# Kernel optimization log

Measured on AMD Instinct MI355X. Metric: run time of the kernel, lower is better.

Reference implementation:

```python
import jax, jax.numpy as jnp
import numpy as np

BSZ, N, E, D = 8, 1024, 49152, 256
K, ALPHA = 10, 0.1
EDGE_RATIO, NODE_RATIO = 0.8, 0.7
K_NODES = int(np.ceil(NODE_RATIO * N))  # torch_geometric topk uses ceil -> 717


def setup_inputs() -> dict:
    key = jax.random.key(0)
    ks = jax.random.split(key, 10)
    concept_hidden = jax.random.normal(ks[0], (BSZ, N, D), jnp.float32)
    head = jax.random.randint(ks[1], (BSZ, E), 0, N, jnp.int32)
    off = jax.random.randint(ks[2], (BSZ, E), 1, N, jnp.int32)
    tail = ((head + off) % N).astype(jnp.int32)  # guaranteed no self-loops
    triple_label = jnp.ones((BSZ, E), jnp.int32)  # all edges valid (no -1 padding)
    relation_hidden = jnp.zeros((BSZ, 1), jnp.float32)  # unused by the math
    concept_labels = jax.random.randint(ks[3], (BSZ, N), 0, 3, jnp.int32)
    concept_ids = jax.random.randint(ks[4], (BSZ, N), 0, 50000, jnp.int32)
    # PageRank temp (learnable param, deterministic init from alpha/K)
    t = ALPHA * (1.0 - ALPHA) ** np.arange(K + 1)
    t[-1] = (1.0 - ALPHA) ** K
    temp = jnp.asarray(t, jnp.float32)
    # GraphAttention params (heads=1)
    g = float(np.sqrt(6.0 / (D + D)))
    W_proj = jax.random.uniform(ks[5], (D, D), jnp.float32, -g, g)
    ga = float(np.sqrt(6.0 / (1 + D)))
    a_src = jax.random.uniform(ks[6], (D,), jnp.float32, -ga, ga)
    a_tgt = jax.random.uniform(ks[7], (D,), jnp.float32, -ga, ga)
    # output Linear(2D -> D)
    gl = float(np.sqrt(1.0 / (2 * D)))
    W_lin = jax.random.uniform(ks[8], (D, 2 * D), jnp.float32, -gl, gl)
    b_lin = jax.random.uniform(ks[9], (D,), jnp.float32, -gl, gl)
    return dict(concept_hidden=concept_hidden, relation_hidden=relation_hidden,
                head=head, tail=tail, triple_label=triple_label,
                concept_labels=concept_labels, concept_ids=concept_ids,
                temp=temp, W_proj=W_proj, a_src=a_src, a_tgt=a_tgt,
                W_lin=W_lin, b_lin=b_lin)


def _per_sample(x, h, t, labels, ids, temp, W_proj, a_src, a_tgt, W_lin, b_lin):
    # ---- PageRank (gcn_norm with added self-loops, aggr='add' into tail) ----
    sl = jnp.arange(N, dtype=jnp.int32)
    hs = jnp.concatenate([h, sl])
    ts = jnp.concatenate([t, sl])
    deg = jax.ops.segment_sum(jnp.ones(E + N, x.dtype), ts, num_segments=N)
    dinv = jnp.where(deg > 0, jax.lax.rsqrt(deg), 0.0)
    norm = dinv[hs] * dinv[ts]  # [E+N]

    def step(xk, gamma):
        xk = jax.ops.segment_sum(norm[:, None] * xk[hs], ts, num_segments=N)
        return xk, gamma * xk

    _, contribs = jax.lax.scan(step, x, temp[1:])  # K steps
    x_cut = temp[0] * x + contribs.sum(0)  # [N, D]

    # ---- edge attention (GAT-style scoring, sigmoid) ----
    proj = x_cut @ W_proj.T                       # [N, D] (heads=1)
    s_src = proj @ a_src                          # [N]
    s_tgt = proj @ a_tgt                          # [N]
    attn = jax.nn.sigmoid(s_src[h] + s_tgt[t])    # [E]

    # ---- symmetrize + coalesce(mean), done densely ----
    rows = jnp.concatenate([h, t])
    cols = jnp.concatenate([t, h])
    vals = jnp.concatenate([attn, attn])
    S = jnp.zeros((N, N), x.dtype).at[rows, cols].add(vals)
    Cn = jnp.zeros((N, N), x.dtype).at[rows, cols].add(1.0)
    valid = Cn > 0
    A = jnp.where(valid, S / jnp.maximum(Cn, 1.0), 0.0)  # coalesced mean adjacency

    # ---- np.percentile(attn, 20) with linear interpolation over valid edges ----
    sv = jnp.sort(jnp.where(valid, A, jnp.inf).reshape(-1))  # valid values first
    M = valid.sum()
    pos = (1.0 - EDGE_RATIO) * (M.astype(x.dtype) - 1.0)
    lo = jnp.floor(pos).astype(jnp.int32)
    frac = pos - lo.astype(x.dtype)
    hi = jnp.minimum(lo + 1, M - 1)  # stays within the finite (valid) prefix
    cut = sv[lo] + frac * (sv[hi] - sv[lo])

    A_cut = jnp.where(valid & (A >= cut), A, 0.0)  # edges below percentile zeroed

    # ---- node scoring: scatter_add of attn*x[src] into dst == A_cut^T @ x ----
    out = A_cut.T @ x                              # [N, D]
    score = jnp.abs(out).sum(1) + 1e-7             # [N]
    _, perm = jax.lax.top_k(score, K_NODES)

    pooled = A_cut[perm] @ x                       # [k, D]
    hcat = jnp.concatenate([x[perm], pooled], axis=-1)  # [k, 2D]
    h_new = hcat @ W_lin.T + b_lin                 # [k, D]
    return h_new, labels[perm], ids[perm]


def reference(concept_hidden, relation_hidden, head, tail, triple_label,
              concept_labels, concept_ids, temp, W_proj, a_src, a_tgt,
              W_lin, b_lin):
    f = jax.vmap(_per_sample,
                 in_axes=(0, 0, 0, 0, 0, None, None, None, None, None, None))
    return f(concept_hidden, head, tail, concept_labels, concept_ids,
             temp, W_proj, a_src, a_tgt, W_lin, b_lin)
```

## Files before the change

kernel.cpp:

```cpp
#include <hip/hip_runtime.h>
#include <math.h>

#define BSZ 8
#define NN 1024
#define EE 49152
#define DD 256
#define KSTEPS 10
#define NCH 192
#define KNODES 717
#define RS 256
#define MROWS 720

typedef __attribute__((ext_vector_type(8))) short short8_t;
typedef __attribute__((ext_vector_type(4))) float f32x4;

__device__ __forceinline__ void fma4(float4& a, float w, const float4 v) {
    a.x += w * v.x; a.y += w * v.y; a.z += w * v.z; a.w += w * v.w;
}

__device__ __forceinline__ unsigned short f2bf(float f) {
    unsigned u = __float_as_uint(f);
    u = (u + 0x7fffu + ((u >> 16) & 1u)) >> 16;
    return (unsigned short)u;
}


__global__ void k_hist(const int* __restrict__ head, const int* __restrict__ tail,
                       int* __restrict__ cnt_t, int* __restrict__ cnt_h) {
    __shared__ int lt[NN];
    __shared__ int lh[NN];
    int b = blockIdx.x / NCH, ch = blockIdx.x % NCH;
    int tid = threadIdx.x;
    for (int i = tid; i < NN; i += 256) { lt[i] = 0; lh[i] = 0; }
    __syncthreads();
    int e = ch * 256 + tid;
    int h = head[b * EE + e], t = tail[b * EE + e];
    atomicAdd(&lt[t], 1);
    atomicAdd(&lh[h], 1);
    __syncthreads();
    int base = (b * NCH + ch) * NN;
    for (int i = tid; i < NN; i += 256) { cnt_t[base + i] = lt[i]; cnt_h[base + i] = lh[i]; }
}

__global__ void k_chunkscan(int* __restrict__ cnt_t, int* __restrict__ cnt_h,
                            int* __restrict__ tot_t, int* __restrict__ tot_h,
                            float* __restrict__ dinv) {
    int gid = blockIdx.x * 256 + threadIdx.x;
    int which = gid >> 13;
    int i = gid & 8191;
    int b = i >> 10, n = i & 1023;
    int* c = which ? cnt_h : cnt_t;
    int run = 0;
    for (int s = 0; s < NCH; s++) {
        int idx = (b * NCH + s) * NN + n;
        int v = c[idx];
        c[idx] = run;
        run += v;
    }
    (which ? tot_h : tot_t)[i] = run;
    if (!which) dinv[i] = 1.0f / sqrtf((float)(run + 1));
}

__global__ __launch_bounds__(1024) void k_nodescan(const int* __restrict__ tot_t,
                                                   const int* __restrict__ tot_h,
                                                   int* __restrict__ toff, int* __restrict__ hoff) {
    __shared__ int sb[NN];
    int b = blockIdx.x >> 1, which = blockIdx.x & 1;
    int tid = threadIdx.x;
    const int* tot = which ? tot_h : tot_t;
    int* off = which ? hoff : toff;
    int v = tot[b * NN + tid];
    sb[tid] = v;
    __syncthreads();
    for (int o = 1; o < NN; o <<= 1) {
        int t = (tid >= o) ? sb[tid - o] : 0;
        __syncthreads();
        sb[tid] += t;
        __syncthreads();
    }
    off[b * (NN + 1) + tid] = sb[tid] - v;
    if (tid == NN - 1) off[b * (NN + 1) + NN] = sb[tid];
}

__global__ void k_fill(const int* __restrict__ head, const int* __restrict__ tail,
                       const int* __restrict__ cnt_t, const int* __restrict__ cnt_h,
                       const int* __restrict__ toff, const int* __restrict__ hoff,
                       const float* __restrict__ dinv,
                       int* __restrict__ t_head, float* __restrict__ t_norm, int* __restrict__ t_eidx,
                       int* __restrict__ h_tail, int* __restrict__ h_eidx) {
    __shared__ int sh[256], st[256];
    int b = blockIdx.x / NCH, ch = blockIdx.x % NCH;
    int tid = threadIdx.x;
    int e = ch * 256 + tid;
    int h = head[b * EE + e], t = tail[b * EE + e];
    sh[tid] = h;
    st[tid] = t;
    __syncthreads();
    int rt = 0, rh = 0;
    for (int j = 0; j < tid; j++) {
        rt += (st[j] == t);
        rh += (sh[j] == h);
    }
    int post = toff[b * (NN + 1) + t] + cnt_t[(b * NCH + ch) * NN + t] + rt;
    t_head[b * EE + post] = h;
    t_norm[b * EE + post] = dinv[b * NN + h] * dinv[b * NN + t];
    t_eidx[b * EE + post] = e;
    int posh = hoff[b * (NN + 1) + h] + cnt_h[(b * NCH + ch) * NN + h] + rh;
    h_tail[b * EE + posh] = t;
    h_eidx[b * EE + posh] = e;
}

__global__ __launch_bounds__(256) void k_prstep(const float* __restrict__ src, float* __restrict__ dst,
                         float* __restrict__ xacc, const float* __restrict__ temp,
                         const int* __restrict__ toff, const int* __restrict__ t_head,
                         const float* __restrict__ t_norm, const float* __restrict__ dinv,
                         int kidx) {
    int wid = threadIdx.x >> 6, lane = threadIdx.x & 63;
    int b = blockIdx.x & 7;
    int n = (blockIdx.x >> 3) * 4 + wid;
    int g = b * NN + n;
    int o0 = __builtin_amdgcn_readfirstlane(toff[b * (NN + 1) + n]);
    int o1 = __builtin_amdgcn_readfirstlane(toff[b * (NN + 1) + n + 1]);
    int ebase = __builtin_amdgcn_readfirstlane(b * EE);
    const int* __restrict__ hp = t_head + ebase;
    const float* __restrict__ wp = t_norm + ebase;
    float dv = dinv[g];
    const float4* src4 = (const float4*)src;
    size_t r4 = (size_t)g * 64 + lane;
    size_t bb = (size_t)b * NN * 64;
    float4 sv = src4[r4];
    float sl = dv * dv;
    float4 acc;
    acc.x = sl * sv.x; acc.y = sl * sv.y; acc.z = sl * sv.z; acc.w = sl * sv.w;
    int j = o0;
    for (; j + 8 <= o1; j += 8) {
        int c0 = hp[j], c1 = hp[j + 1], c2 = hp[j + 2], c3 = hp[j + 3];
        int c4 = hp[j + 4], c5 = hp[j + 5], c6 = hp[j + 6], c7 = hp[j + 7];
        float w0 = wp[j], w1 = wp[j + 1], w2 = wp[j + 2], w3 = wp[j + 3];
        float w4 = wp[j + 4], w5 = wp[j + 5], w6 = wp[j + 6], w7 = wp[j + 7];
        float4 xa = src4[bb + (size_t)c0 * 64 + lane];
        float4 xb = src4[bb + (size_t)c1 * 64 + lane];
        float4 xc = src4[bb + (size_t)c2 * 64 + lane];
        float4 xd = src4[bb + (size_t)c3 * 64 + lane];
        float4 xe = src4[bb + (size_t)c4 * 64 + lane];
        float4 xf = src4[bb + (size_t)c5 * 64 + lane];
        float4 xg = src4[bb + (size_t)c6 * 64 + lane];
        float4 xh = src4[bb + (size_t)c7 * 64 + lane];
        fma4(acc, w0, xa); fma4(acc, w1, xb); fma4(acc, w2, xc); fma4(acc, w3, xd);
        fma4(acc, w4, xe); fma4(acc, w5, xf); fma4(acc, w6, xg); fma4(acc, w7, xh);
    }
    for (; j + 4 <= o1; j += 4) {
        int c0 = hp[j], c1 = hp[j + 1], c2 = hp[j + 2], c3 = hp[j + 3];
        float w0 = wp[j], w1 = wp[j + 1], w2 = wp[j + 2], w3 = wp[j + 3];
        float4 xa = src4[bb + (size_t)c0 * 64 + lane];
        float4 xb = src4[bb + (size_t)c1 * 64 + lane];
        float4 xc = src4[bb + (size_t)c2 * 64 + lane];
        float4 xd = src4[bb + (size_t)c3 * 64 + lane];
        fma4(acc, w0, xa); fma4(acc, w1, xb); fma4(acc, w2, xc); fma4(acc, w3, xd);
    }
    for (; j < o1; j++) {
        int c0 = hp[j];
        float w0 = wp[j];
        float4 xa = src4[bb + (size_t)c0 * 64 + lane];
        fma4(acc, w0, xa);
    }
    ((float4*)dst)[r4] = acc;
    float gm = temp[kidx + 1];
    float4 xa2;
    if (kidx == 0) {
        float t0 = temp[0];
        xa2.x = t0 * sv.x; xa2.y = t0 * sv.y; xa2.z = t0 * sv.z; xa2.w = t0 * sv.w;
    } else {
        xa2 = ((float4*)xacc)[r4];
    }
    fma4(xa2, gm, acc);
    ((float4*)xacc)[r4] = xa2;
}


__global__ void k_vsrc(const float* __restrict__ Wp, const float* __restrict__ as_,
                       const float* __restrict__ at_, float* __restrict__ vsrc,
                       float* __restrict__ vtgt) {
    int d = threadIdx.x;
    float vs = 0.f, vt = 0.f;
    for (int i = 0; i < DD; i++) {
        float w = Wp[i * DD + d];
        vs += as_[i] * w;
        vt += at_[i] * w;
    }
    vsrc[d] = vs;
    vtgt[d] = vt;
}

__global__ void k_s(const float* __restrict__ xacc, const float* __restrict__ vsrc,
                    const float* __restrict__ vtgt, float* __restrict__ ssrc,
                    float* __restrict__ stgt) {
    int g = blockIdx.x * 4 + (threadIdx.x >> 6);
    int lane = threadIdx.x & 63;
    const float4* xr = (const float4*)(xacc + (size_t)g * DD);
    float4 xv = xr[lane];
    float4 vs = ((const float4*)vsrc)[lane];
    float4 vt = ((const float4*)vtgt)[lane];
    float s1 = xv.x * vs.x + xv.y * vs.y + xv.z * vs.z + xv.w * vs.w;
    float s2 = xv.x * vt.x + xv.y * vt.y + xv.z * vt.z + xv.w * vt.w;
    for (int o = 32; o > 0; o >>= 1) {
        s1 += __shfl_down(s1, o);
        s2 += __shfl_down(s2, o);
    }
    if (lane == 0) {
        ssrc[g] = s1;
        stgt[g] = s2;
    }
}

__global__ void k_attn(const int* __restrict__ head, const int* __restrict__ tail,
                       const float* __restrict__ ssrc, const float* __restrict__ stgt,
                       float* __restrict__ attn) {
    int i = blockIdx.x * 256 + threadIdx.x;
    int b = i / EE;
    int h = head[i], t = tail[i];
    float z = ssrc[b * NN + h] + stgt[b * NN + t];
    attn[i] = 1.0f / (1.0f + expf(-z));
}


__global__ __launch_bounds__(256) void k_rowbuild(const int* __restrict__ hoff, const int* __restrict__ h_tail,
                          const int* __restrict__ h_eidx, const int* __restrict__ toff,
                          const int* __restrict__ t_head, const int* __restrict__ t_eidx,
                          const float* __restrict__ attn,
                          int* __restrict__ rcol, float* __restrict__ rval,
                          int* __restrict__ nnzrow) {
    __shared__ int cols[RS];
    __shared__ float vals[RS];
    __shared__ int first[NN];
    __shared__ int cntb[NN];
    __shared__ int rankv[NN];
    __shared__ int ssum[256];
    int g = blockIdx.x;
    int b = g >> 10, n = g & 1023;
    int tid = threadIdx.x;
    int a0 = hoff[b * (NN + 1) + n], a1 = hoff[b * (NN + 1) + n + 1];
    int c0 = toff[b * (NN + 1) + n], c1 = toff[b * (NN + 1) + n + 1];
    int kh = a1 - a0;
    int kk = kh + (c1 - c0);
    if (kk > RS) kk = RS;
    for (int i = tid; i < NN; i += 256) { first[i] = 0x7fffffff; cntb[i] = 0; }
    __syncthreads();
    if (tid < kk) {
        int c, e;
        if (tid < kh) { c = h_tail[b * EE + a0 + tid]; e = h_eidx[b * EE + a0 + tid]; }
        else          { c = t_head[b * EE + c0 + (tid - kh)]; e = t_eidx[b * EE + c0 + (tid - kh)]; }
        cols[tid] = c;
        vals[tid] = attn[b * EE + e];
        atomicMin(&first[c], tid);
        atomicAdd(&cntb[c], 1);
    }
    __syncthreads();
    int i0 = tid * 4;
    int p0 = (first[i0] != 0x7fffffff);
    int p1 = (first[i0 + 1] != 0x7fffffff);
    int p2 = (first[i0 + 2] != 0x7fffffff);
    int p3 = (first[i0 + 3] != 0x7fffffff);
    int psum = p0 + p1 + p2 + p3;
    ssum[tid] = psum;
    __syncthreads();
    for (int o = 1; o < 256; o <<= 1) {
        int t = (tid >= o) ? ssum[tid - o] : 0;
        __syncthreads();
        ssum[tid] += t;
        __syncthreads();
    }
    int run = ssum[tid] - psum;
    rankv[i0] = run;            run += p0;
    rankv[i0 + 1] = run;        run += p1;
    rankv[i0 + 2] = run;        run += p2;
    rankv[i0 + 3] = run;
    int total = ssum[255];
    __syncthreads();
    if (tid < kk) {
        int c = cols[tid];
        if (first[c] == tid) {
            int cc = cntb[c];
            float v;
            if (cc == 1) {
                v = vals[tid];
            } else {
                float s = 0.f;
                for (int j = tid; j < kk; j++)
                    if (cols[j] == c) s += vals[j];
                v = s / (float)cc;
            }
            size_t rb = ((size_t)g << 8) + rankv[c];
            rcol[rb] = c;
            rval[rb] = v;
        }
    }
    if (tid == 0) nnzrow[g] = total;
}

__global__ void k_msum(const int* __restrict__ nnzrow, int* __restrict__ Mcnt) {
    __shared__ int red[256];
    int b = blockIdx.x, tid = threadIdx.x;
    int s = nnzrow[b * NN + tid] + nnzrow[b * NN + 256 + tid] +
            nnzrow[b * NN + 512 + tid] + nnzrow[b * NN + 768 + tid];
    red[tid] = s;
    __syncthreads();
    for (int o = 128; o > 0; o >>= 1) {
        if (tid < o) red[tid] += red[tid + o];
        __syncthreads();
    }
    if (tid == 0) Mcnt[b] = red[0];
}


__global__ void k_selinit(const int* __restrict__ Mcnt, int* __restrict__ sel) {
    int b = threadIdx.x;
    if (b < BSZ) {
        int M = Mcnt[b];
        float pos = 0.2f * ((float)M - 1.0f);
        int lo = (int)floorf(pos);
        float frac = pos - (float)lo;
        sel[b * 8 + 0] = lo;
        sel[b * 8 + 1] = min(lo + 1, M - 1);
        sel[b * 8 + 2] = 0;
        sel[b * 8 + 3] = 0;
        sel[b * 8 + 4] = __float_as_int(frac);
    }
}

__global__ void k_selhist(const float* __restrict__ rv, const int* __restrict__ sel,
                          int* __restrict__ hist, int pass) {
    __shared__ int lh[512];
    int tid = threadIdx.x;
    lh[tid] = 0;
    lh[tid + 256] = 0;
    __syncthreads();
    size_t base = (size_t)blockIdx.x * 1024;
    int b = blockIdx.x >> 8;
    unsigned p0 = (unsigned)sel[b * 8 + 2];
    unsigned p1 = (unsigned)sel[b * 8 + 3];
    int shift = 24 - 8 * pass;
    for (int u = 0; u < 4; u++) {
        float a = rv[base + u * 256 + tid];
        if (a > 0.f) {
            unsigned bits = __float_as_uint(a);
            unsigned bucket = (bits >> shift) & 255u;
            if (pass == 0) {
                atomicAdd(&lh[bucket], 1);
                atomicAdd(&lh[256 + bucket], 1);
            } else {
                unsigned hibits = bits >> (shift + 8);
                if (hibits == p0) atomicAdd(&lh[bucket], 1);
                if (hibits == p1) atomicAdd(&lh[256 + bucket], 1);
            }
        }
    }
    __syncthreads();
    int v0 = lh[tid];
    if (v0) atomicAdd(&hist[(b * 2 + 0) * 256 + tid], v0);
    int v1 = lh[tid + 256];
    if (v1) atomicAdd(&hist[(b * 2 + 1) * 256 + tid], v1);
}

__global__ void k_selreduce(int* __restrict__ hist, int* __restrict__ sel) {
    __shared__ int sb[256];
    int b = blockIdx.x >> 1, ch = blockIdx.x & 1;
    int tid = threadIdx.x;
    int idx = (b * 2 + ch) * 256 + tid;
    int v = hist[idx];
    hist[idx] = 0;
    int rem = sel[b * 8 + ch];
    int pref = sel[b * 8 + 2 + ch];
    sb[tid] = v;
    __syncthreads();
    for (int o = 1; o < 256; o <<= 1) {
        int t = (tid >= o) ? sb[tid - o] : 0;
        __syncthreads();
        sb[tid] += t;
        __syncthreads();
    }
    int excl = sb[tid] - v;
    if (v > 0 && rem >= excl && rem < excl + v) {
        sel[b * 8 + ch] = rem - excl;
        sel[b * 8 + 2 + ch] = (pref << 8) | tid;
    }
}

__global__ void k_cut(const int* __restrict__ sel, float* __restrict__ cut) {
    int b = threadIdx.x;
    if (b < BSZ) {
        float v0 = __uint_as_float((unsigned)sel[b * 8 + 2]);
        float v1 = __uint_as_float((unsigned)sel[b * 8 + 3]);
        float frac = __int_as_float(sel[b * 8 + 4]);
        cut[b] = v0 + frac * (v1 - v0);
    }
}


__global__ __launch_bounds__(256) void k_outscore(const int* __restrict__ rcol, const float* __restrict__ rval,
                           const int* __restrict__ nnzrow, const float* __restrict__ x,
                           const float* __restrict__ cut, float* __restrict__ out_pr,
                           float* __restrict__ score) {
    int wid = threadIdx.x >> 6, lane = threadIdx.x & 63;
    int b = blockIdx.x & 7;
    int n = (blockIdx.x >> 3) * 4 + wid;
    int g = b * NN + n;
    float cb = cut[b];
    int nnz = __builtin_amdgcn_readfirstlane(nnzrow[g]);
    int rbase = __builtin_amdgcn_readfirstlane(g << 8);
    const int* __restrict__ cp = rcol + rbase;
    const float* __restrict__ vp = rval + rbase;
    const float4* x4 = (const float4*)x;
    size_t bb = (size_t)b * NN * 64;
    float4 acc = make_float4(0.f, 0.f, 0.f, 0.f);
    int j = 0;
    for (; j + 4 <= nnz; j += 4) {
        float a0 = vp[j], a1 = vp[j + 1], a2 = vp[j + 2], a3 = vp[j + 3];
        int c0 = cp[j], c1 = cp[j + 1], c2 = cp[j + 2], c3 = cp[j + 3];
        float4 xa = x4[bb + (size_t)c0 * 64 + lane];
        float4 xb = x4[bb + (size_t)c1 * 64 + lane];
        float4 xc = x4[bb + (size_t)c2 * 64 + lane];
        float4 xd = x4[bb + (size_t)c3 * 64 + lane];
        if (a0 >= cb) fma4(acc, a0, xa);
        if (a1 >= cb) fma4(acc, a1, xb);
        if (a2 >= cb) fma4(acc, a2, xc);
        if (a3 >= cb) fma4(acc, a3, xd);
    }
    for (; j < nnz; j++) {
        float a0 = vp[j];
        int c0 = cp[j];
        float4 xa = x4[bb + (size_t)c0 * 64 + lane];
        if (a0 >= cb) fma4(acc, a0, xa);
    }
    ((float4*)out_pr)[(size_t)g * 64 + lane] = acc;
    float4 r;
    r.x = fabsf(acc.x); r.y = fabsf(acc.y); r.z = fabsf(acc.z); r.w = fabsf(acc.w);
    for (int o = 32; o > 0; o >>= 1) {
        r.x += __shfl_down(r.x, o);
        r.y += __shfl_down(r.y, o);
        r.z += __shfl_down(r.z, o);
        r.w += __shfl_down(r.w, o);
    }
    r.x += r.z;
    r.y += r.w;
    r.x += r.y;
    if (lane == 0) score[g] = r.x + 1e-7f;
}


__global__ __launch_bounds__(1024) void k_topk(const float* __restrict__ score,
                                               const int* __restrict__ labels,
                                               const int* __restrict__ ids,
                                               int* __restrict__ perm,
                                               float* __restrict__ out_lab,
                                               float* __restrict__ out_ids) {
    __shared__ float sc[NN];
    __shared__ int idx[NN];
    int b = blockIdx.x, tid = threadIdx.x;
    sc[tid] = score[b * NN + tid];
    idx[tid] = tid;
    __syncthreads();
    for (int k = 2; k <= NN; k <<= 1) {
        for (int j = k >> 1; j > 0; j >>= 1) {
            int p = tid ^ j;
            if (p > tid) {
                float s0 = sc[tid], s1 = sc[p];
                int i0 = idx[tid], i1 = idx[p];
                bool before01 = (s0 > s1) || (s0 == s1 && i0 < i1);
                bool up = ((tid & k) == 0);
                bool sw = up ? (!before01) : before01;
                if (sw) {
                    sc[tid] = s1; sc[p] = s0;
                    idx[tid] = i1; idx[p] = i0;
                }
            }
            __syncthreads();
        }
    }
    perm[b * NN + tid] = idx[tid];
    if (tid < KNODES) {
        int p = idx[tid];
        out_lab[b * KNODES + tid] = (float)labels[b * NN + p];
        out_ids[b * KNODES + tid] = (float)ids[b * NN + p];
    }
}


__global__ void k_wbf16(const float* __restrict__ W, unsigned short* __restrict__ Wb) {
    int i = blockIdx.x * 256 + threadIdx.x;
    Wb[i] = f2bf(W[i]);
}

__global__ void k_packA(const float* __restrict__ x, const float* __restrict__ outpr,
                        const int* __restrict__ perm, unsigned short* __restrict__ A16) {
    int row = blockIdx.x;
    int b = row / MROWS, i = row - b * MROWS;
    int tid = threadIdx.x;
    size_t ob = (size_t)row * 512;
    if (i < KNODES) {
        int p = perm[b * NN + i];
        float v0 = x[((size_t)(b * NN + p)) * DD + tid];
        float v1 = outpr[((size_t)(b * NN + p)) * DD + tid];
        A16[ob + tid] = f2bf(v0);
        A16[ob + 256 + tid] = f2bf(v1);
    } else {
        A16[ob + tid] = 0;
        A16[ob + 256 + tid] = 0;
    }
}

__global__ __launch_bounds__(256) void k_hnew_mfma(const unsigned short* __restrict__ A16,
                                                   const unsigned short* __restrict__ Wb,
                                                   const float* __restrict__ b_lin,
                                                   float* __restrict__ hnew) {
    int w = blockIdx.x * 4 + (threadIdx.x >> 6);
    int lane = threadIdx.x & 63;
    int b = w / (45 * 16);
    int rem = w - b * (45 * 16);
    int mt = rem >> 4, nt = rem & 15;
    int m = lane & 15, quad = lane >> 4;
    const unsigned short* ap = A16 + ((size_t)(b * MROWS + mt * 16 + m) * 512 + quad * 8);
    const unsigned short* bp = Wb + ((size_t)(nt * 16 + m) * 512 + quad * 8);
    f32x4 acc = {0.f, 0.f, 0.f, 0.f};
#pragma unroll
    for (int s = 0; s < 16; s++) {
        short8_t av = *(const short8_t*)(ap + s * 32);
        short8_t bv = *(const short8_t*)(bp + s * 32);
        acc = __builtin_amdgcn_mfma_f32_16x16x32_bf16(av, bv, acc, 0, 0, 0);
    }
    int d = nt * 16 + m;
    float bl = b_lin[d];
#pragma unroll
    for (int r = 0; r < 4; r++) {
        int i = mt * 16 + quad * 4 + r;
        if (i < KNODES) hnew[((size_t)(b * KNODES + i)) * DD + d] = acc[r] + bl;
    }
}


extern "C" void kernel_launch(void* const* d_in, const int* in_sizes, int n_in,
                              void* d_out, int out_size, void* d_ws, size_t ws_size,
                              hipStream_t stream) {
    const float* x      = (const float*)d_in[0];
    const int*   head   = (const int*)d_in[2];
    const int*   tail   = (const int*)d_in[3];
    const int*   labels = (const int*)d_in[5];
    const int*   ids    = (const int*)d_in[6];
    const float* temp   = (const float*)d_in[7];
    const float* Wp     = (const float*)d_in[8];
    const float* asrc   = (const float*)d_in[9];
    const float* atgt   = (const float*)d_in[10];
    const float* Wl     = (const float*)d_in[11];
    const float* blin   = (const float*)d_in[12];

    float* out_h   = (float*)d_out;
    float* out_lab = out_h + (size_t)BSZ * KNODES * DD;
    float* out_ids = out_lab + (size_t)BSZ * KNODES;

    size_t o = 0;
    char* ws = (char*)d_ws;
    auto A_ = [&](size_t bytes) -> void* {
        void* p = ws + o;
        o += (bytes + 255) & ~(size_t)255;
        return p;
    };
    int*   cnt_t  = (int*)  A_((size_t)BSZ * NCH * NN * 4);
    int*   cnt_h  = (int*)  A_((size_t)BSZ * NCH * NN * 4);
    int*   tot_t  = (int*)  A_((size_t)BSZ * NN * 4);
    int*   tot_h  = (int*)  A_((size_t)BSZ * NN * 4);
    int*   toff   = (int*)  A_((size_t)BSZ * (NN + 1) * 4);
    int*   hoff   = (int*)  A_((size_t)BSZ * (NN + 1) * 4);
    float* dinv   = (float*)A_((size_t)BSZ * NN * 4);
    int*   t_head = (int*)  A_((size_t)BSZ * EE * 4);
    float* t_norm = (float*)A_((size_t)BSZ * EE * 4);
    int*   t_eidx = (int*)  A_((size_t)BSZ * EE * 4);
    int*   h_tail = (int*)  A_((size_t)BSZ * EE * 4);
    int*   h_eidx = (int*)  A_((size_t)BSZ * EE * 4);
    float* xkA    = (float*)A_((size_t)BSZ * NN * DD * 4);
    float* xkB    = (float*)A_((size_t)BSZ * NN * DD * 4);
    float* xacc   = (float*)A_((size_t)BSZ * NN * DD * 4);
    float* vsrc   = (float*)A_(DD * 4);
    float* vtgt   = (float*)A_(DD * 4);
    float* ssrc   = (float*)A_((size_t)BSZ * NN * 4);
    float* stgt   = (float*)A_((size_t)BSZ * NN * 4);
    float* attn   = (float*)A_((size_t)BSZ * EE * 4);
    int*   rcol   = (int*)  A_((size_t)BSZ * NN * RS * 4);
    float* rval   = (float*)A_((size_t)BSZ * NN * RS * 4);
    int*   nnzrow = (int*)  A_((size_t)BSZ * NN * 4);
    int*   Mcnt   = (int*)  A_(BSZ * 4);
    int*   sel    = (int*)  A_(BSZ * 8 * 4);
    int*   hist   = (int*)  A_(BSZ * 2 * 256 * 4);
    float* cutv   = (float*)A_(BSZ * 4);
    float* outpr  = (float*)A_((size_t)BSZ * NN * DD * 4);
    float* scorev = (float*)A_((size_t)BSZ * NN * 4);
    int*   perm   = (int*)  A_((size_t)BSZ * NN * 4);
    unsigned short* Wb16 = (unsigned short*)A_((size_t)DD * 512 * 2);
    unsigned short* A16  = (unsigned short*)A_((size_t)BSZ * MROWS * 512 * 2);
    if (o > ws_size) return;

    hipMemsetAsync(rval, 0, (size_t)BSZ * NN * RS * 4, stream);
    hipMemsetAsync(hist, 0, BSZ * 2 * 256 * 4, stream);

    k_wbf16<<<DD * 512 / 256, 256, 0, stream>>>(Wl, Wb16);
    k_hist<<<BSZ * NCH, 256, 0, stream>>>(head, tail, cnt_t, cnt_h);
    k_chunkscan<<<64, 256, 0, stream>>>(cnt_t, cnt_h, tot_t, tot_h, dinv);
    k_nodescan<<<16, 1024, 0, stream>>>(tot_t, tot_h, toff, hoff);
    k_fill<<<BSZ * NCH, 256, 0, stream>>>(head, tail, cnt_t, cnt_h, toff, hoff, dinv,
                                          t_head, t_norm, t_eidx, h_tail, h_eidx);
    for (int k = 0; k < KSTEPS; k++) {
        const float* src = (k == 0) ? x : ((k & 1) ? xkA : xkB);
        float* dst = (k & 1) ? xkB : xkA;
        k_prstep<<<BSZ * NN / 4, 256, 0, stream>>>(src, dst, xacc, temp, toff, t_head, t_norm, dinv, k);
    }
    k_vsrc<<<1, 256, 0, stream>>>(Wp, asrc, atgt, vsrc, vtgt);
    k_s<<<BSZ * NN / 4, 256, 0, stream>>>(xacc, vsrc, vtgt, ssrc, stgt);
    k_attn<<<BSZ * EE / 256, 256, 0, stream>>>(head, tail, ssrc, stgt, attn);
    k_rowbuild<<<BSZ * NN, 256, 0, stream>>>(hoff, h_tail, h_eidx, toff, t_head, t_eidx,
                                             attn, rcol, rval, nnzrow);
    k_msum<<<BSZ, 256, 0, stream>>>(nnzrow, Mcnt);
    k_selinit<<<1, 64, 0, stream>>>(Mcnt, sel);
    for (int p = 0; p < 4; p++) {
        k_selhist<<<BSZ * 256, 256, 0, stream>>>(rval, sel, hist, p);
        k_selreduce<<<16, 256, 0, stream>>>(hist, sel);
    }
    k_cut<<<1, 64, 0, stream>>>(sel, cutv);
    k_outscore<<<BSZ * NN / 4, 256, 0, stream>>>(rcol, rval, nnzrow, x, cutv, outpr, scorev);
    k_topk<<<BSZ, 1024, 0, stream>>>(scorev, labels, ids, perm, out_lab, out_ids);
    k_packA<<<BSZ * MROWS, 256, 0, stream>>>(x, outpr, perm, A16);
    k_hnew_mfma<<<BSZ * 45 * 16 / 4, 256, 0, stream>>>(A16, Wb16, blin, out_h);
}
```

Before: 465.3 us.

## Fuse small kernels, compact percentile values, single-kernel radix select, fuse packA into topk

Folds the W_lin bf16 conversion into k_hist and the vsrc computation into the last PageRank step as extra blocks. k_rowbuild now appends each row's values to a compact per-batch buffer through an atomic base. This lets one block-per-batch k_select replace the msum/selinit/4×(selhist+selreduce)/cut launch chain and removes the large rval memset. The PR gather loop is unrolled to 16, and A16 packing moves into k_topk. It saves many launches and the full rval scans, but the select and packing now run on only 8 blocks, which limits parallelism.

```diff
diff --git a/kernel.cpp b/kernel.cpp
--- a/kernel.cpp
+++ b/kernel.cpp
@@ -10,6 +10,7 @@
 #define KNODES 717
 #define RS 256
 #define MROWS 720
+#define CSTRIDE 131072
 
 typedef __attribute__((ext_vector_type(8))) short short8_t;
 typedef __attribute__((ext_vector_type(4))) float f32x4;
@@ -26,11 +27,17 @@
 
 
 __global__ void k_hist(const int* __restrict__ head, const int* __restrict__ tail,
-                       int* __restrict__ cnt_t, int* __restrict__ cnt_h) {
+                       int* __restrict__ cnt_t, int* __restrict__ cnt_h,
+                       const float* __restrict__ Wl, unsigned short* __restrict__ Wb) {
     __shared__ int lt[NN];
     __shared__ int lh[NN];
+    int tid = threadIdx.x;
+    if (blockIdx.x >= BSZ * NCH) {
+        int i = (blockIdx.x - BSZ * NCH) * 256 + tid;
+        Wb[i] = f2bf(Wl[i]);
+        return;
+    }
     int b = blockIdx.x / NCH, ch = blockIdx.x % NCH;
-    int tid = threadIdx.x;
     for (int i = tid; i < NN; i += 256) { lt[i] = 0; lh[i] = 0; }
     __syncthreads();
     int e = ch * 256 + tid;
@@ -114,7 +121,22 @@
                          float* __restrict__ xacc, const float* __restrict__ temp,
                          const int* __restrict__ toff, const int* __restrict__ t_head,
                          const float* __restrict__ t_norm, const float* __restrict__ dinv,
-                         int kidx) {
+                         int kidx,
+                         const float* __restrict__ Wp, const float* __restrict__ as_,
+                         const float* __restrict__ at_, float* __restrict__ vsrc,
+                         float* __restrict__ vtgt) {
+    if (blockIdx.x >= BSZ * NN / 4) {
+        int d = threadIdx.x;
+        float vs = 0.f, vt = 0.f;
+        for (int i = 0; i < DD; i++) {
+            float w = Wp[i * DD + d];
+            vs += as_[i] * w;
+            vt += at_[i] * w;
+        }
+        vsrc[d] = vs;
+        vtgt[d] = vt;
+        return;
+    }
     int wid = threadIdx.x >> 6, lane = threadIdx.x & 63;
     int b = blockIdx.x & 7;
     int n = (blockIdx.x >> 3) * 4 + wid;
@@ -133,21 +155,17 @@
     float4 acc;
     acc.x = sl * sv.x; acc.y = sl * sv.y; acc.z = sl * sv.z; acc.w = sl * sv.w;
     int j = o0;
-    for (; j + 8 <= o1; j += 8) {
-        int c0 = hp[j], c1 = hp[j + 1], c2 = hp[j + 2], c3 = hp[j + 3];
-        int c4 = hp[j + 4], c5 = hp[j + 5], c6 = hp[j + 6], c7 = hp[j + 7];
-        float w0 = wp[j], w1 = wp[j + 1], w2 = wp[j + 2], w3 = wp[j + 3];
-        float w4 = wp[j + 4], w5 = wp[j + 5], w6 = wp[j + 6], w7 = wp[j + 7];
-        float4 xa = src4[bb + (size_t)c0 * 64 + lane];
-        float4 xb = src4[bb + (size_t)c1 * 64 + lane];
-        float4 xc = src4[bb + (size_t)c2 * 64 + lane];
-        float4 xd = src4[bb + (size_t)c3 * 64 + lane];
-        float4 xe = src4[bb + (size_t)c4 * 64 + lane];
-        float4 xf = src4[bb + (size_t)c5 * 64 + lane];
-        float4 xg = src4[bb + (size_t)c6 * 64 + lane];
-        float4 xh = src4[bb + (size_t)c7 * 64 + lane];
-        fma4(acc, w0, xa); fma4(acc, w1, xb); fma4(acc, w2, xc); fma4(acc, w3, xd);
-        fma4(acc, w4, xe); fma4(acc, w5, xf); fma4(acc, w6, xg); fma4(acc, w7, xh);
+    for (; j + 16 <= o1; j += 16) {
+        float wv[16];
+        float4 xv[16];
+#pragma unroll
+        for (int u = 0; u < 16; u++) {
+            int c = hp[j + u];
+            wv[u] = wp[j + u];
+            xv[u] = src4[bb + (size_t)c * 64 + lane];
+        }
+#pragma unroll
+        for (int u = 0; u < 16; u++) fma4(acc, wv[u], xv[u]);
     }
     for (; j + 4 <= o1; j += 4) {
         int c0 = hp[j], c1 = hp[j + 1], c2 = hp[j + 2], c3 = hp[j + 3];
@@ -177,20 +195,6 @@
     ((float4*)xacc)[r4] = xa2;
 }
 
-
-__global__ void k_vsrc(const float* __restrict__ Wp, const float* __restrict__ as_,
-                       const float* __restrict__ at_, float* __restrict__ vsrc,
-                       float* __restrict__ vtgt) {
-    int d = threadIdx.x;
-    float vs = 0.f, vt = 0.f;
-    for (int i = 0; i < DD; i++) {
-        float w = Wp[i * DD + d];
-        vs += as_[i] * w;
-        vt += at_[i] * w;
-    }
-    vsrc[d] = vs;
-    vtgt[d] = vt;
-}
 
 __global__ void k_s(const float* __restrict__ xacc, const float* __restrict__ vsrc,
                     const float* __restrict__ vtgt, float* __restrict__ ssrc,
@@ -229,13 +233,15 @@
                           const int* __restrict__ t_head, const int* __restrict__ t_eidx,
                           const float* __restrict__ attn,
                           int* __restrict__ rcol, float* __restrict__ rval,
-                          int* __restrict__ nnzrow) {
+                          int* __restrict__ nnzrow,
+                          float* __restrict__ cvals, int* __restrict__ ccount) {
     __shared__ int cols[RS];
     __shared__ float vals[RS];
     __shared__ int first[NN];
     __shared__ int cntb[NN];
     __shared__ int rankv[NN];
     __shared__ int ssum[256];
+    __shared__ int cbase;
     int g = blockIdx.x;
     int b = g >> 10, n = g & 1023;
     int tid = threadIdx.x;
@@ -276,6 +282,7 @@
     rankv[i0 + 2] = run;        run += p2;
     rankv[i0 + 3] = run;
     int total = ssum[255];
+    if (tid == 0) cbase = atomicAdd(&ccount[b], total);
     __syncthreads();
     if (tid < kk) {
         int c = cols[tid];
@@ -290,109 +297,74 @@
                     if (cols[j] == c) s += vals[j];
                 v = s / (float)cc;
             }
-            size_t rb = ((size_t)g << 8) + rankv[c];
+            int r = rankv[c];
+            size_t rb = ((size_t)g << 8) + r;
             rcol[rb] = c;
             rval[rb] = v;
+            cvals[(size_t)b * CSTRIDE + cbase + r] = v;
         }
     }
     if (tid == 0) nnzrow[g] = total;
 }
 
-__global__ void k_msum(const int* __restrict__ nnzrow, int* __restrict__ Mcnt) {
-    __shared__ int red[256];
-    int b = blockIdx.x, tid = threadIdx.x;
-    int s = nnzrow[b * NN + tid] + nnzrow[b * NN + 256 + tid] +
-            nnzrow[b * NN + 512 + tid] + nnzrow[b * NN + 768 + tid];
-    red[tid] = s;
-    __syncthreads();
-    for (int o = 128; o > 0; o >>= 1) {
-        if (tid < o) red[tid] += red[tid + o];
-        __syncthreads();
-    }
-    if (tid == 0) Mcnt[b] = red[0];
-}
-
-
-__global__ void k_selinit(const int* __restrict__ Mcnt, int* __restrict__ sel) {
-    int b = threadIdx.x;
-    if (b < BSZ) {
-        int M = Mcnt[b];
+
+__global__ __launch_bounds__(1024) void k_select(const float* __restrict__ cvals,
+                                                 const int* __restrict__ ccount,
+                                                 float* __restrict__ cutv) {
+    __shared__ int lh[512];
+    __shared__ int state[5];
+    int b = blockIdx.x;
+    int tid = threadIdx.x;
+    int M = ccount[b];
+    if (tid == 0) {
         float pos = 0.2f * ((float)M - 1.0f);
         int lo = (int)floorf(pos);
         float frac = pos - (float)lo;
-        sel[b * 8 + 0] = lo;
-        sel[b * 8 + 1] = min(lo + 1, M - 1);
-        sel[b * 8 + 2] = 0;
-        sel[b * 8 + 3] = 0;
-        sel[b * 8 + 4] = __float_as_int(frac);
-    }
-}
-
-__global__ void k_selhist(const float* __restrict__ rv, const int* __restrict__ sel,
-                          int* __restrict__ hist, int pass) {
-    __shared__ int lh[512];
-    int tid = threadIdx.x;
-    lh[tid] = 0;
-    lh[tid + 256] = 0;
-    __syncthreads();
-    size_t base = (size_t)blockIdx.x * 1024;
-    int b = blockIdx.x >> 8;
-    unsigned p0 = (unsigned)sel[b * 8 + 2];
-    unsigned p1 = (unsigned)sel[b * 8 + 3];
-    int shift = 24 - 8 * pass;
-    for (int u = 0; u < 4; u++) {
-        float a = rv[base + u * 256 + tid];
-        if (a > 0.f) {
-            unsigned bits = __float_as_uint(a);
+        state[0] = lo;
+        state[1] = min(lo + 1, M - 1);
+        state[2] = 0;
+        state[3] = 0;
+        state[4] = __float_as_int(frac);
+    }
+    const float* vp = cvals + (size_t)b * CSTRIDE;
+    for (int pass = 0; pass < 4; pass++) {
+        if (tid < 512) lh[tid] = 0;
+        __syncthreads();
+        unsigned p0 = (unsigned)state[2];
+        unsigned p1 = (unsigned)state[3];
+        int shift = 24 - 8 * pass;
+        for (int i = tid; i < M; i += 1024) {
+            unsigned bits = __float_as_uint(vp[i]);
             unsigned bucket = (bits >> shift) & 255u;
             if (pass == 0) {
                 atomicAdd(&lh[bucket], 1);
                 atomicAdd(&lh[256 + bucket], 1);
             } else {
-                unsigned hibits = bits >> (shift + 8);
-                if (hibits == p0) atomicAdd(&lh[bucket], 1);
-                if (hibits == p1) atomicAdd(&lh[256 + bucket], 1);
+                unsigned hb = bits >> (shift + 8);
+                if (hb == p0) atomicAdd(&lh[bucket], 1);
+                if (hb == p1) atomicAdd(&lh[256 + bucket], 1);
             }
         }
-    }
-    __syncthreads();
-    int v0 = lh[tid];
-    if (v0) atomicAdd(&hist[(b * 2 + 0) * 256 + tid], v0);
-    int v1 = lh[tid + 256];
-    if (v1) atomicAdd(&hist[(b * 2 + 1) * 256 + tid], v1);
-}
-
-__global__ void k_selreduce(int* __restrict__ hist, int* __restrict__ sel) {
-    __shared__ int sb[256];
-    int b = blockIdx.x >> 1, ch = blockIdx.x & 1;
-    int tid = threadIdx.x;
-    int idx = (b * 2 + ch) * 256 + tid;
-    int v = hist[idx];
-    hist[idx] = 0;
-    int rem = sel[b * 8 + ch];
-    int pref = sel[b * 8 + 2 + ch];
-    sb[tid] = v;
-    __syncthreads();
-    for (int o = 1; o < 256; o <<= 1) {
-        int t = (tid >= o) ? sb[tid - o] : 0;
-        __syncthreads();
-        sb[tid] += t;
-        __syncthreads();
-    }
-    int excl = sb[tid] - v;
-    if (v > 0 && rem >= excl && rem < excl + v) {
-        sel[b * 8 + ch] = rem - excl;
-        sel[b * 8 + 2 + ch] = (pref << 8) | tid;
-    }
-}
-
-__global__ void k_cut(const int* __restrict__ sel, float* __restrict__ cut) {
-    int b = threadIdx.x;
-    if (b < BSZ) {
-        float v0 = __uint_as_float((unsigned)sel[b * 8 + 2]);
-        float v1 = __uint_as_float((unsigned)sel[b * 8 + 3]);
-        float frac = __int_as_float(sel[b * 8 + 4]);
-        cut[b] = v0 + frac * (v1 - v0);
+        __syncthreads();
+        if (tid < 2) {
+            int rem = state[tid];
+            int pref = state[2 + tid];
+            int run2 = 0, selb = 0, selrem = 0;
+            for (int k2 = 0; k2 < 256; k2++) {
+                int v = lh[tid * 256 + k2];
+                if (rem >= run2 && rem < run2 + v) { selb = k2; selrem = rem - run2; }
+                run2 += v;
+            }
+            state[tid] = selrem;
+            state[2 + tid] = (pref << 8) | selb;
+        }
+        __syncthreads();
+    }
+    if (tid == 0) {
+        float v0 = __uint_as_float((unsigned)state[2]);
+        float v1 = __uint_as_float((unsigned)state[3]);
+        float frac = __int_as_float(state[4]);
+        cutv[b] = v0 + frac * (v1 - v0);
     }
 }
 
@@ -451,9 +423,11 @@
 __global__ __launch_bounds__(1024) void k_topk(const float* __restrict__ score,
                                                const int* __restrict__ labels,
                                                const int* __restrict__ ids,
-                                               int* __restrict__ perm,
+                                               const float* __restrict__ x,
+                                               const float* __restrict__ outpr,
                                                float* __restrict__ out_lab,
-                                               float* __restrict__ out_ids) {
+                                               float* __restrict__ out_ids,
+                                               unsigned short* __restrict__ A16) {
     __shared__ float sc[NN];
     __shared__ int idx[NN];
     int b = blockIdx.x, tid = threadIdx.x;
@@ -477,35 +451,22 @@
             __syncthreads();
         }
     }
-    perm[b * NN + tid] = idx[tid];
     if (tid < KNODES) {
         int p = idx[tid];
         out_lab[b * KNODES + tid] = (float)labels[b * NN + p];
         out_ids[b * KNODES + tid] = (float)ids[b * NN + p];
     }
-}
-
-
-__global__ void k_wbf16(const float* __restrict__ W, unsigned short* __restrict__ Wb) {
-    int i = blockIdx.x * 256 + threadIdx.x;
-    Wb[i] = f2bf(W[i]);
-}
-
-__global__ void k_packA(const float* __restrict__ x, const float* __restrict__ outpr,
-                        const int* __restrict__ perm, unsigned short* __restrict__ A16) {
-    int row = blockIdx.x;
-    int b = row / MROWS, i = row - b * MROWS;
-    int tid = threadIdx.x;
-    size_t ob = (size_t)row * 512;
-    if (i < KNODES) {
-        int p = perm[b * NN + i];
-        float v0 = x[((size_t)(b * NN + p)) * DD + tid];
-        float v1 = outpr[((size_t)(b * NN + p)) * DD + tid];
-        A16[ob + tid] = f2bf(v0);
-        A16[ob + 256 + tid] = f2bf(v1);
-    } else {
-        A16[ob + tid] = 0;
-        A16[ob + 256 + tid] = 0;
+    unsigned short* ab = A16 + (size_t)b * MROWS * 512;
+    for (int q = tid; q < MROWS * 512; q += 1024) {
+        int i = q >> 9, c = q & 511;
+        unsigned short v = 0;
+        if (i < KNODES) {
+            int p = idx[i];
+            size_t base = ((size_t)(b * NN + p)) * DD;
+            float f = (c < DD) ? x[base + c] : outpr[base + (c - DD)];
+            v = f2bf(f);
+        }
+        ab[q] = v;
     }
 }
 
@@ -587,22 +548,18 @@
     int*   rcol   = (int*)  A_((size_t)BSZ * NN * RS * 4);
     float* rval   = (float*)A_((size_t)BSZ * NN * RS * 4);
     int*   nnzrow = (int*)  A_((size_t)BSZ * NN * 4);
-    int*   Mcnt   = (int*)  A_(BSZ * 4);
-    int*   sel    = (int*)  A_(BSZ * 8 * 4);
-    int*   hist   = (int*)  A_(BSZ * 2 * 256 * 4);
+    float* cvals  = (float*)A_((size_t)BSZ * CSTRIDE * 4);
+    int*   ccount = (int*)  A_(BSZ * 4);
     float* cutv   = (float*)A_(BSZ * 4);
     float* outpr  = (float*)A_((size_t)BSZ * NN * DD * 4);
     float* scorev = (float*)A_((size_t)BSZ * NN * 4);
-    int*   perm   = (int*)  A_((size_t)BSZ * NN * 4);
     unsigned short* Wb16 = (unsigned short*)A_((size_t)DD * 512 * 2);
     unsigned short* A16  = (unsigned short*)A_((size_t)BSZ * MROWS * 512 * 2);
     if (o > ws_size) return;
 
-    hipMemsetAsync(rval, 0, (size_t)BSZ * NN * RS * 4, stream);
-    hipMemsetAsync(hist, 0, BSZ * 2 * 256 * 4, stream);
-
-    k_wbf16<<<DD * 512 / 256, 256, 0, stream>>>(Wl, Wb16);
-    k_hist<<<BSZ * NCH, 256, 0, stream>>>(head, tail, cnt_t, cnt_h);
+    hipMemsetAsync(ccount, 0, BSZ * 4, stream);
+
+    k_hist<<<BSZ * NCH + 512, 256, 0, stream>>>(head, tail, cnt_t, cnt_h, Wl, Wb16);
     k_chunkscan<<<64, 256, 0, stream>>>(cnt_t, cnt_h, tot_t, tot_h, dinv);
     k_nodescan<<<16, 1024, 0, stream>>>(tot_t, tot_h, toff, hoff);
     k_fill<<<BSZ * NCH, 256, 0, stream>>>(head, tail, cnt_t, cnt_h, toff, hoff, dinv,
@@ -610,22 +567,16 @@
     for (int k = 0; k < KSTEPS; k++) {
         const float* src = (k == 0) ? x : ((k & 1) ? xkA : xkB);
         float* dst = (k & 1) ? xkB : xkA;
-        k_prstep<<<BSZ * NN / 4, 256, 0, stream>>>(src, dst, xacc, temp, toff, t_head, t_norm, dinv, k);
-    }
-    k_vsrc<<<1, 256, 0, stream>>>(Wp, asrc, atgt, vsrc, vtgt);
+        int grid = BSZ * NN / 4 + ((k == KSTEPS - 1) ? 1 : 0);
+        k_prstep<<<grid, 256, 0, stream>>>(src, dst, xacc, temp, toff, t_head, t_norm, dinv, k,
+                                           Wp, asrc, atgt, vsrc, vtgt);
+    }
     k_s<<<BSZ * NN / 4, 256, 0, stream>>>(xacc, vsrc, vtgt, ssrc, stgt);
     k_attn<<<BSZ * EE / 256, 256, 0, stream>>>(head, tail, ssrc, stgt, attn);
     k_rowbuild<<<BSZ * NN, 256, 0, stream>>>(hoff, h_tail, h_eidx, toff, t_head, t_eidx,
-                                             attn, rcol, rval, nnzrow);
-    k_msum<<<BSZ, 256, 0, stream>>>(nnzrow, Mcnt);
-    k_selinit<<<1, 64, 0, stream>>>(Mcnt, sel);
-    for (int p = 0; p < 4; p++) {
-        k_selhist<<<BSZ * 256, 256, 0, stream>>>(rval, sel, hist, p);
-        k_selreduce<<<16, 256, 0, stream>>>(hist, sel);
-    }
-    k_cut<<<1, 64, 0, stream>>>(sel, cutv);
+                                             attn, rcol, rval, nnzrow, cvals, ccount);
+    k_select<<<BSZ, 1024, 0, stream>>>(cvals, ccount, cutv);
     k_outscore<<<BSZ * NN / 4, 256, 0, stream>>>(rcol, rval, nnzrow, x, cutv, outpr, scorev);
-    k_topk<<<BSZ, 1024, 0, stream>>>(scorev, labels, ids, perm, out_lab, out_ids);
-    k_packA<<<BSZ * MROWS, 256, 0, stream>>>(x, outpr, perm, A16);
+    k_topk<<<BSZ, 1024, 0, stream>>>(scorev, labels, ids, x, outpr, out_lab, out_ids, A16);
     k_hnew_mfma<<<BSZ * 45 * 16 / 4, 256, 0, stream>>>(A16, Wb16, blin, out_h);
 }
```

Measured after the change: 829.8 us. 78.4% more time.
